# Kernel optimization log

Hardware: AMD Instinct MI355X
Metric: run time of the kernel (lower is better)

## Reference

```python
import jax, jax.numpy as jnp
import numpy as np


def setup_inputs() -> dict:
    key = jax.random.key(0)
    k1, k2, k3 = jax.random.split(key, 3)
    N, P, D = 4, 1024, 1024
    E, H = 8, 2048
    sequences = jax.random.normal(k1, (N, P, D), dtype=jnp.float32)
    # torch Linear layout: weight [out, in]
    gate_W = jax.random.normal(k2, (E, D), dtype=jnp.float32) * (1.0 / np.sqrt(D))
    gate_b = jnp.zeros((E,), dtype=jnp.float32)
    # xavier_uniform bound for Linear(D, H)
    bound = float(np.sqrt(6.0 / (D + H)))
    expert_W = jax.random.uniform(k3, (E, H, D), dtype=jnp.float32, minval=-bound, maxval=bound)
    expert_b = jnp.zeros((E, H), dtype=jnp.float32)
    return {"sequences": sequences, "gate_W": gate_W, "gate_b": gate_b,
            "expert_W": expert_W, "expert_b": expert_b, "moe_top_k": 2}


def reference(sequences, gate_W, gate_b, expert_W, expert_b, moe_top_k):
    N, P, D = sequences.shape
    E = expert_W.shape[0]
    x = sequences.reshape(-1, D)                       # [T, D]
    gating_scores = jax.nn.softmax(x @ gate_W.T + gate_b, axis=-1)  # [T, E]
    _, top_k_idx = jax.lax.top_k(gating_scores, moe_top_k)          # [T, k]
    # boolean dispatch mask: token t routed to expert e (topk indices are unique)
    mask = jax.nn.one_hot(top_k_idx, E, dtype=x.dtype).sum(axis=1)  # [T, E] in {0,1}
    out = jnp.zeros((x.shape[0], expert_W.shape[1]), dtype=x.dtype)
    # loop over small fixed expert set; masked dense GEMM per expert
    for e in range(E):
        out = out + mask[:, e:e + 1] * (x @ expert_W[e].T + expert_b[e])
    # NOTE: original adds UNWEIGHTED expert outputs, then divides by top_k
    out = out / moe_top_k
    gating_variances = jnp.var(gating_scores, axis=0, ddof=1)  # torch.var unbiased
    return out.reshape(N, P, -1), gating_variances
```

## Files before the change

kernel.cpp:

```cpp
#include <hip/hip_runtime.h>


#define NTOK 4096
#define DIM  1024
#define NEXP 8
#define HID  2048

#define BM 128
#define BN 128
#define BK 64

using u16    = unsigned short;
using u16x4  = __attribute__((ext_vector_type(4))) unsigned short;
using u16x8  = __attribute__((ext_vector_type(8))) unsigned short;
using bf16x8 = __attribute__((ext_vector_type(8))) __bf16;
using f32x4  = __attribute__((ext_vector_type(4))) float;

typedef const __attribute__((address_space(1))) unsigned char* gas1p;
typedef __attribute__((address_space(3))) unsigned char* gas3p;

__device__ __forceinline__ void gload16(void* lds, const void* g) {
  __builtin_amdgcn_global_load_lds((gas1p)g, (gas3p)lds, 16, 0, 0);
}

__device__ inline u16 f2bf(float f) {
  union { float f; unsigned u; } v; v.f = f;
  unsigned r = v.u + 0x7fffu + ((v.u >> 16) & 1u);
  return (u16)(r >> 16);
}
__device__ inline float bf2f(u16 b) {
  union { unsigned u; float f; } v; v.u = ((unsigned)b) << 16; return v.f;
}

__global__ __launch_bounds__(256) void convert_bf16(
    const float* __restrict__ in, u16* __restrict__ out) {
  int i = blockIdx.x * 256 + threadIdx.x;
  const float4* p = (const float4*)in + (size_t)i * 2;
  float4 a = p[0], b = p[1];
  u16x8 r;
  r[0] = f2bf(a.x); r[1] = f2bf(a.y); r[2] = f2bf(a.z); r[3] = f2bf(a.w);
  r[4] = f2bf(b.x); r[5] = f2bf(b.y); r[6] = f2bf(b.z); r[7] = f2bf(b.w);
  *((u16x8*)out + i) = r;
}

__global__ __launch_bounds__(256) void gate_kernel(
    const float* __restrict__ x, const float* __restrict__ gW,
    const float* __restrict__ gb, float* __restrict__ probs,
    int* __restrict__ top2, u16* __restrict__ xbf) {
  const int wave = threadIdx.x >> 6;
  const int lane = threadIdx.x & 63;
  const int t = blockIdx.x * 4 + wave;

  const float4* xrow = (const float4*)(x + (size_t)t * DIM);
  double acc[NEXP];
#pragma unroll
  for (int e = 0; e < NEXP; ++e) acc[e] = 0.0;

#pragma unroll
  for (int c = 0; c < 4; ++c) {
    int idx = c * 64 + lane;
    float4 xv = xrow[idx];
    u16x4 bv;
    bv[0] = f2bf(xv.x); bv[1] = f2bf(xv.y); bv[2] = f2bf(xv.z); bv[3] = f2bf(xv.w);
    *(u16x4*)(xbf + (size_t)t * DIM + 4 * idx) = bv;
#pragma unroll
    for (int e = 0; e < NEXP; ++e) {
      float4 wv = ((const float4*)(gW + (size_t)e * DIM))[idx];
      acc[e] += (double)xv.x * wv.x + (double)xv.y * wv.y +
                (double)xv.z * wv.z + (double)xv.w * wv.w;
    }
  }
#pragma unroll
  for (int e = 0; e < NEXP; ++e) {
    double v = acc[e];
#pragma unroll
    for (int off = 32; off > 0; off >>= 1) v += __shfl_down(v, off);
    acc[e] = v;
  }

  if (lane == 0) {
    double logits[NEXP];
#pragma unroll
    for (int e = 0; e < NEXP; ++e) logits[e] = acc[e] + (double)gb[e];
    double m = logits[0];
#pragma unroll
    for (int e = 1; e < NEXP; ++e) m = fmax(m, logits[e]);
    double p[NEXP], s = 0.0;
#pragma unroll
    for (int e = 0; e < NEXP; ++e) { p[e] = exp(logits[e] - m); s += p[e]; }
#pragma unroll
    for (int e = 0; e < NEXP; ++e) p[e] /= s;

    int i1 = 0;
#pragma unroll
    for (int e = 1; e < NEXP; ++e) if (p[e] > p[i1]) i1 = e;
    int i2 = (i1 == 0) ? 1 : 0;
#pragma unroll
    for (int e = 0; e < NEXP; ++e) {
      if (e != i1 && p[e] > p[i2]) i2 = e;
    }

#pragma unroll
    for (int e = 0; e < NEXP; ++e) probs[(size_t)t * NEXP + e] = (float)p[e];
    top2[t] = i1 | (i2 << 4);
  }
}

__global__ __launch_bounds__(256) void route_kernel(
    const float* __restrict__ probs, const int* __restrict__ top2,
    int* __restrict__ counts, int* __restrict__ lists,
    float* __restrict__ var_out) {
  const int e = blockIdx.x;
  const int tid = threadIdx.x;
  const int lane = tid & 63;
  const int wave = tid >> 6;

  __shared__ int wsum[4];
  __shared__ double ds[4], dq[4];

  double s = 0.0, q = 0.0;
  int base = 0;

  for (int c = 0; c < NTOK / 256; ++c) {
    int t = c * 256 + tid;
    float p = probs[(size_t)t * NEXP + e];
    s += (double)p;
    q += (double)p * (double)p;

    int m = top2[t];
    bool f = ((m & 15) == e) || (((m >> 4) & 15) == e);
    unsigned long long bal = __ballot(f);
    int before = __popcll(bal & ((1ull << lane) - 1ull));
    if (lane == 0) wsum[wave] = __popcll(bal);
    __syncthreads();
    int woff = 0;
#pragma unroll
    for (int w = 0; w < 4; ++w) if (w < wave) woff += wsum[w];
    int ctotal = wsum[0] + wsum[1] + wsum[2] + wsum[3];
    if (f) lists[e * NTOK + base + woff + before] = t;
    base += ctotal;
    __syncthreads();
  }
  if (tid == 0) counts[e] = base;

#pragma unroll
  for (int off = 32; off > 0; off >>= 1) {
    s += __shfl_down(s, off);
    q += __shfl_down(q, off);
  }
  if (lane == 0) { ds[wave] = s; dq[wave] = q; }
  __syncthreads();
  if (tid == 0) {
    double S = ds[0] + ds[1] + ds[2] + ds[3];
    double Q = dq[0] + dq[1] + dq[2] + dq[3];
    var_out[e] = (float)((Q - S * S / (double)NTOK) / (double)(NTOK - 1));
  }
}

__global__ __launch_bounds__(256, 4) void expert_gemm(
    const u16* __restrict__ xbf, const u16* __restrict__ wbf,
    const float* __restrict__ eb, const int* __restrict__ counts,
    const int* __restrict__ lists, const int* __restrict__ top2,
    u16* __restrict__ pbf) {
  __shared__ u16 As[BM * BK];
  __shared__ u16 Bs[BN * BK];
  __shared__ int tok[BM];
  __shared__ int kslot[BM];

  const int bid = (blockIdx.x & 7) * (4096 / 8) + (blockIdx.x >> 3);

  const int e  = bid >> 9;
  const int rb = (bid >> 4) & 31;
  const int cb = bid & 15;
  const int cnt = counts[e];
  if (rb * BM >= cnt) return;

  const int tid  = threadIdx.x;
  const int wave = tid >> 6;
  const int lane = tid & 63;

  if (tid < BM) {
    int gi = rb * BM + tid;
    int tr = (gi < cnt) ? lists[e * NTOK + gi] : -1;
    tok[tid] = tr;
    kslot[tid] = (tr >= 0 && (top2[tr] & 15) == e) ? 0 : 1;
  }
  __syncthreads();

  const u16* asrc[4];
  const u16* bsrc[4];
  int ldsoff[4];
#pragma unroll
  for (int j = 0; j < 4; ++j) {
    const int idx  = (j * 4 + wave) * 64 + lane;
    const int row  = idx >> 3;
    const int c16  = (idx & 7) ^ (row & 7);
    int tr = tok[row]; if (tr < 0) tr = 0;
    asrc[j] = xbf + (size_t)tr * DIM + c16 * 8;
    bsrc[j] = wbf + ((size_t)e * HID + (size_t)cb * BN + row) * DIM + c16 * 8;
    ldsoff[j] = (j * 4 + wave) * 512;
  }

  const int wm = (wave >> 1) * 64;
  const int wn = (wave & 1) * 64;
  const int lr = lane & 15;
  const int hk = lane >> 4;

  f32x4 acc[4][4];
#pragma unroll
  for (int m = 0; m < 4; ++m)
#pragma unroll
    for (int n = 0; n < 4; ++n) acc[m][n] = (f32x4)(0.0f);

  for (int k0 = 0; k0 < DIM; k0 += BK) {
#pragma unroll
    for (int j = 0; j < 4; ++j) gload16(&As[ldsoff[j]], asrc[j] + k0);
#pragma unroll
    for (int j = 0; j < 4; ++j) gload16(&Bs[ldsoff[j]], bsrc[j] + k0);

    __syncthreads();

    bf16x8 fa[2][4], fb[2][4];
#pragma unroll
    for (int kk = 0; kk < 2; ++kk) {
#pragma unroll
      for (int m = 0; m < 4; ++m) {
        const int row = wm + m * 16 + lr;
        const int c16 = (kk * 4 + hk) ^ (row & 7);
        fa[kk][m] = *(const bf16x8*)&As[row * 64 + c16 * 8];
      }
#pragma unroll
      for (int n = 0; n < 4; ++n) {
        const int row = wn + n * 16 + lr;
        const int c16 = (kk * 4 + hk) ^ (row & 7);
        fb[kk][n] = *(const bf16x8*)&Bs[row * 64 + c16 * 8];
      }
    }

#pragma unroll
    for (int kk = 0; kk < 2; ++kk)
#pragma unroll
      for (int m = 0; m < 4; ++m)
#pragma unroll
        for (int n = 0; n < 4; ++n)
          acc[m][n] = __builtin_amdgcn_mfma_f32_16x16x32_bf16(
              fa[kk][m], fb[kk][n], acc[m][n], 0, 0, 0);

    __syncthreads();
  }

#pragma unroll
  for (int n = 0; n < 4; ++n) {
    const int hcol = cb * BN + wn + n * 16 + lr;
#pragma unroll
    for (int m = 0; m < 4; ++m) {
#pragma unroll
      for (int i = 0; i < 4; ++i) {
        int rloc = wm + m * 16 + hk * 4 + i;
        int tr = tok[rloc];
        if (tr >= 0)
          pbf[((size_t)kslot[rloc] * NTOK + tr) * HID + hcol] =
              f2bf(acc[m][n][i]);
      }
    }
  }
}

__global__ __launch_bounds__(256) void combine_kernel(
    const u16* __restrict__ pbf, const int* __restrict__ top2,
    const float* __restrict__ eb, float* __restrict__ out) {
  const int t = blockIdx.x;
  const int h = threadIdx.x * 8;
  const int m2 = top2[t];
  const int e1 = m2 & 15, e2 = (m2 >> 4) & 15;

  u16x8 p0 = *(const u16x8*)&pbf[(size_t)t * HID + h];
  u16x8 p1 = *(const u16x8*)&pbf[((size_t)NTOK + t) * HID + h];
  const float4* b1 = (const float4*)&eb[e1 * HID + h];
  const float4* b2 = (const float4*)&eb[e2 * HID + h];
  float4 b1a = b1[0], b1b = b1[1], b2a = b2[0], b2b = b2[1];

  float4 o0, o1;
  o0.x = 0.5f * (bf2f(p0[0]) + bf2f(p1[0]) + b1a.x + b2a.x);
  o0.y = 0.5f * (bf2f(p0[1]) + bf2f(p1[1]) + b1a.y + b2a.y);
  o0.z = 0.5f * (bf2f(p0[2]) + bf2f(p1[2]) + b1a.z + b2a.z);
  o0.w = 0.5f * (bf2f(p0[3]) + bf2f(p1[3]) + b1a.w + b2a.w);
  o1.x = 0.5f * (bf2f(p0[4]) + bf2f(p1[4]) + b1b.x + b2b.x);
  o1.y = 0.5f * (bf2f(p0[5]) + bf2f(p1[5]) + b1b.y + b2b.y);
  o1.z = 0.5f * (bf2f(p0[6]) + bf2f(p1[6]) + b1b.z + b2b.z);
  o1.w = 0.5f * (bf2f(p0[7]) + bf2f(p1[7]) + b1b.w + b2b.w);

  float4* po = (float4*)&out[(size_t)t * HID + h];
  po[0] = o0; po[1] = o1;
}

extern "C" void kernel_launch(void* const* d_in, const int* in_sizes, int n_in,
                              void* d_out, int out_size, void* d_ws, size_t ws_size,
                              hipStream_t stream) {
  const float* x  = (const float*)d_in[0];
  const float* gW = (const float*)d_in[1];
  const float* gb = (const float*)d_in[2];
  const float* eW = (const float*)d_in[3];
  const float* eb = (const float*)d_in[4];

  float* out = (float*)d_out;
  float* var_out = out + (size_t)NTOK * HID;

  char* ws = (char*)d_ws;
  int*   counts = (int*)ws;
  int*   lists  = (int*)(ws + 1024);
  float* probs  = (float*)(ws + 1024 + 131072);
  int*   top2   = (int*)(ws + 1024 + 2 * 131072);
  u16*   xbf    = (u16*)(ws + 294912);
  u16*   wbf    = (u16*)((char*)xbf + (size_t)NTOK * DIM * 2);
  u16*   pbf    = (u16*)((char*)wbf + (size_t)NEXP * HID * DIM * 2);

  convert_bf16<<<(NEXP * HID * DIM) / (256 * 8), 256, 0, stream>>>(eW, wbf);
  gate_kernel<<<NTOK / 4, 256, 0, stream>>>(x, gW, gb, probs, top2, xbf);
  route_kernel<<<NEXP, 256, 0, stream>>>(probs, top2, counts, lists, var_out);
  expert_gemm<<<NEXP * (NTOK / BM) * (HID / BN), 256, 0, stream>>>(
      xbf, wbf, eb, counts, lists, top2, pbf);
  combine_kernel<<<NTOK, 256, 0, stream>>>(pbf, top2, eb, out);
}
```

Baseline: 132.8 us.

## Double-buffer LDS tiles in expert GEMM with explicit vmcnt waits

Converts the expert GEMM main loop to a two-stage LDS double buffer: the next two K tiles are prefetched with direct-to-LDS global loads, and each iteration waits only on the older tile's loads using s_waitcnt vmcnt before a raw barrier. The aim is to overlap global memory latency with MFMA work instead of stalling at every tile. LDS use doubles and launch bounds drop to 2 blocks per CU, which lowers occupancy. The XCD-swizzled block index mapping is also removed, changing cache locality across dies, and the unused bias argument is dropped.

Result: faster. 117.8 us (-11.3%).

```diff
diff --git a/kernel.cpp b/kernel.cpp
--- a/kernel.cpp
+++ b/kernel.cpp
@@ -9,6 +9,7 @@
 #define BM 128
 #define BN 128
 #define BK 64
+#define NT (DIM / BK)
 
 using u16    = unsigned short;
 using u16x4  = __attribute__((ext_vector_type(4))) unsigned short;
@@ -157,18 +158,16 @@
   }
 }
 
-__global__ __launch_bounds__(256, 4) void expert_gemm(
+__global__ __launch_bounds__(256, 2) void expert_gemm(
     const u16* __restrict__ xbf, const u16* __restrict__ wbf,
-    const float* __restrict__ eb, const int* __restrict__ counts,
-    const int* __restrict__ lists, const int* __restrict__ top2,
-    u16* __restrict__ pbf) {
-  __shared__ u16 As[BM * BK];
-  __shared__ u16 Bs[BN * BK];
+    const int* __restrict__ counts, const int* __restrict__ lists,
+    const int* __restrict__ top2, u16* __restrict__ pbf) {
+  __shared__ u16 As[2][BM * BK];
+  __shared__ u16 Bs[2][BN * BK];
   __shared__ int tok[BM];
   __shared__ int kslot[BM];
 
-  const int bid = (blockIdx.x & 7) * (4096 / 8) + (blockIdx.x >> 3);
-
+  const int bid = blockIdx.x;
   const int e  = bid >> 9;
   const int rb = (bid >> 4) & 31;
   const int cb = bid & 15;
@@ -201,6 +200,14 @@
     ldsoff[j] = (j * 4 + wave) * 512;
   }
 
+#define STAGE(buf, k0)                                                        \
+  do {                                                                        \
+    _Pragma("unroll")                                                         \
+    for (int j = 0; j < 4; ++j) gload16(&As[buf][ldsoff[j]], asrc[j] + (k0)); \
+    _Pragma("unroll")                                                         \
+    for (int j = 0; j < 4; ++j) gload16(&Bs[buf][ldsoff[j]], bsrc[j] + (k0)); \
+  } while (0)
+
   const int wm = (wave >> 1) * 64;
   const int wn = (wave & 1) * 64;
   const int lr = lane & 15;
@@ -212,13 +219,17 @@
 #pragma unroll
     for (int n = 0; n < 4; ++n) acc[m][n] = (f32x4)(0.0f);
 
-  for (int k0 = 0; k0 < DIM; k0 += BK) {
-#pragma unroll
-    for (int j = 0; j < 4; ++j) gload16(&As[ldsoff[j]], asrc[j] + k0);
-#pragma unroll
-    for (int j = 0; j < 4; ++j) gload16(&Bs[ldsoff[j]], bsrc[j] + k0);
-
-    __syncthreads();
+  STAGE(0, 0);
+  STAGE(1, BK);
+
+  int cur = 0;
+  for (int kt = 0; kt < NT; ++kt) {
+    if (kt + 1 < NT) {
+      asm volatile("s_waitcnt vmcnt(8)" ::: "memory");
+    } else {
+      asm volatile("s_waitcnt vmcnt(0)" ::: "memory");
+    }
+    __builtin_amdgcn_s_barrier();
 
     bf16x8 fa[2][4], fb[2][4];
 #pragma unroll
@@ -227,13 +238,13 @@
       for (int m = 0; m < 4; ++m) {
         const int row = wm + m * 16 + lr;
         const int c16 = (kk * 4 + hk) ^ (row & 7);
-        fa[kk][m] = *(const bf16x8*)&As[row * 64 + c16 * 8];
+        fa[kk][m] = *(const bf16x8*)&As[cur][row * 64 + c16 * 8];
       }
 #pragma unroll
       for (int n = 0; n < 4; ++n) {
         const int row = wn + n * 16 + lr;
         const int c16 = (kk * 4 + hk) ^ (row & 7);
-        fb[kk][n] = *(const bf16x8*)&Bs[row * 64 + c16 * 8];
+        fb[kk][n] = *(const bf16x8*)&Bs[cur][row * 64 + c16 * 8];
       }
     }
 
@@ -246,8 +257,11 @@
           acc[m][n] = __builtin_amdgcn_mfma_f32_16x16x32_bf16(
               fa[kk][m], fb[kk][n], acc[m][n], 0, 0, 0);
 
-    __syncthreads();
-  }
+    __builtin_amdgcn_s_barrier();
+    if (kt + 2 < NT) STAGE(cur, (kt + 2) * BK);
+    cur ^= 1;
+  }
+#undef STAGE
 
 #pragma unroll
   for (int n = 0; n < 4; ++n) {
@@ -319,6 +333,6 @@
   gate_kernel<<<NTOK / 4, 256, 0, stream>>>(x, gW, gb, probs, top2, xbf);
   route_kernel<<<NEXP, 256, 0, stream>>>(probs, top2, counts, lists, var_out);
   expert_gemm<<<NEXP * (NTOK / BM) * (HID / BN), 256, 0, stream>>>(
-      xbf, wbf, eb, counts, lists, top2, pbf);
+      xbf, wbf, counts, lists, top2, pbf);
   combine_kernel<<<NTOK, 256, 0, stream>>>(pbf, top2, eb, out);
 }
```
